# Kernel optimization log

Measured on AMD Instinct MI355X. Metric: run time of the kernel, lower is better.

## Reference

```python
import jax, jax.numpy as jnp
import numpy as np

N, M = 65536, 512
CTRL = 128
IN_DIM = 128
READ_LEN = M + 6          # [M,1,1,3,1]
WRITE_LEN = 3 * M + 6     # [M,1,1,3,1,M,M]
EPS = 1e-16


def setup_inputs() -> dict:
    key = jax.random.key(0)
    ks = jax.random.split(key, 12)
    s = 0.02
    return {
        "x":   jax.random.normal(ks[0], (4, IN_DIM), jnp.float32),
        "mem": jax.random.normal(ks[1], (N, M), jnp.float32) * 0.05,
        "Wc":  jax.random.normal(ks[2], (CTRL, IN_DIM), jnp.float32) * s,
        "bc":  jnp.zeros((CTRL,), jnp.float32),
        "Wr":  jax.random.normal(ks[3], (READ_LEN, CTRL), jnp.float32) * s,
        "br":  jnp.zeros((READ_LEN,), jnp.float32),
        "Ww":  jax.random.normal(ks[4], (WRITE_LEN, CTRL), jnp.float32) * s,
        "bw":  jnp.zeros((WRITE_LEN,), jnp.float32),
        "W1":  jax.random.normal(ks[5], (200, M + CTRL), jnp.float32) * s,
        "b1":  jnp.zeros((200,), jnp.float32),
        "W2":  jax.random.normal(ks[6], (10, 200), jnp.float32) * s,
        "b2":  jnp.zeros((10,), jnp.float32),
    }


def _address(mem, k, beta, g, s, gamma, w_prev):
    # content + gate + circular shift + sharpen (standard NTM addressing)
    beta = jax.nn.softplus(beta)
    g = jax.nn.sigmoid(g)
    s = jax.nn.softmax(s)                      # (3,)
    gamma = 1.0 + jax.nn.softplus(gamma)
    # cosine similarity against all N memory rows
    dot = mem @ k                              # (N,)
    norms = jnp.sqrt(jnp.sum(mem * mem, axis=1)) * jnp.sqrt(jnp.sum(k * k)) + EPS
    wc = jax.nn.softmax(beta * dot / norms)    # content weights (N,)
    wg = g * wc + (1.0 - g) * w_prev           # gated
    # circular convolution with 3-tap shift kernel s = [s(-1), s(0), s(+1)]
    ws = s[0] * jnp.roll(wg, 1) + s[1] * wg + s[2] * jnp.roll(wg, -1)
    w = ws ** gamma                            # sharpen
    return w / (jnp.sum(w) + EPS)


def _forward(x, mem, Wc, bc, Wr, br, Ww, bw, W1, b1, W2, b2):
    cont = x @ Wc.T + bc                       # controller: (4, 128)
    w0 = jnp.full((N,), 1.0 / N, x.dtype)      # softmax of constant -> uniform

    def step(carry, c_t):
        mem, w_r, w_w = carry
        # ---- write head ----
        ow = c_t @ Ww.T + bw                   # (3M+6,)
        k, b, g, s, y = ow[:M], ow[M], ow[M+1], ow[M+2:M+5], ow[M+5]
        e, a = ow[M+6:2*M+6], ow[2*M+6:]
        w_w = _address(mem, k, b, g, s, y, w_w)
        e = jax.nn.sigmoid(e)
        mem = mem * (1.0 - jnp.outer(w_w, e)) + jnp.outer(w_w, a)
        # ---- read head ----
        orr = c_t @ Wr.T + br                  # (M+6,)
        k, b, g, s, y = orr[:M], orr[M], orr[M+1], orr[M+2:M+5], orr[M+5]
        w_r = _address(mem, k, b, g, s, y, w_r)
        r = w_r @ mem                          # (M,)
        # ---- output MLP ----
        h = jax.nn.relu(jnp.concatenate([c_t, r]) @ W1.T + b1)
        out = h @ W2.T + b2                    # (10,)
        return (mem, w_r, w_w), out

    _, outs = jax.lax.scan(step, (mem, w0, w0), cont)
    return outs                                # (4, 10)


def reference(x, mem, Wc, bc, Wr, br, Ww, bw, W1, b1, W2, b2):
    return _forward(x, mem, Wc, bc, Wr, br, Ww, bw, W1, b1, W2, b2)
```

## Files before the change

kernel.cpp:

```cpp
#include <hip/hip_runtime.h>
#include <hip/hip_cooperative_groups.h>
#include <math.h>

namespace cg = cooperative_groups;

#define NN    65536
#define CTRLD 128
#define WLEN  1542
#define RLEN  518
#define EPSF  1e-16f
#define GRIDB 1024
#define ROWSB 64
#define RPWV  16

typedef float vf2 __attribute__((ext_vector_type(2)));

struct KP {
  const float* mem0; const float* cont;
  unsigned* mem8;
  const float* kW; const float* sW; const float* eW; const float* aW;
  const float* kR; const float* sR; float* kn;
  float *dotR, *dotW, *n2v;
  float *wunW, *pSW, *wunR, *pSR;
  float *pZr, *pZw;
  float *rp, *p2, *hbuf;
  const float *W1, *b1, *W2, *b2;
  float* out;
  const float *x, *Wc, *bc, *Ww, *bw, *Wr, *br;
  float *contw, *kWw, *sWw, *eWw, *aWw, *kRw, *sRw;
};

struct SmemAll {
  float red[256];
  float big[1280];
  float zsh[4][2];
  unsigned m8[ROWSB*128];
};

__device__ __forceinline__ float softplusf_(float x){
    return x > 0.f ? x + log1pf(expf(-x)) : log1pf(expf(x));
}
__device__ __forceinline__ float sigmoidf_(float x){ return 1.f/(1.f+expf(-x)); }
__device__ __forceinline__ float dot4_(const float4& a, const float4& b){
    return a.x*b.x + a.y*b.y + a.z*b.z + a.w*b.w;
}

__device__ __forceinline__ float blockReduce256(float v, float* red){
    int t = threadIdx.x;
    red[t] = v; __syncthreads();
    for(int s = 128; s; s >>= 1){ if(t < s) red[t] += red[t+s]; __syncthreads(); }
    float r = red[0]; __syncthreads();
    return r;
}
__device__ __forceinline__ void waveReduce3(float& a, float& b, float& c){
    for(int o = 32; o; o >>= 1){
        a += __shfl_down(a,o); b += __shfl_down(b,o); c += __shfl_down(c,o);
    }
}
__device__ __forceinline__ void waveReduce1(float& a){
    for(int o = 32; o; o >>= 1) a += __shfl_down(a,o);
}

__device__ __forceinline__ void quant8(const float4& v0, const float4& v1,
                                       unsigned& q0, unsigned& q1){
    int a = __builtin_amdgcn_cvt_pk_fp8_f32(v0.x*64.f, v0.y*64.f, 0, false);
    a     = __builtin_amdgcn_cvt_pk_fp8_f32(v0.z*64.f, v0.w*64.f, a, true);
    int b = __builtin_amdgcn_cvt_pk_fp8_f32(v1.x*64.f, v1.y*64.f, 0, false);
    b     = __builtin_amdgcn_cvt_pk_fp8_f32(v1.z*64.f, v1.w*64.f, b, true);
    q0 = (unsigned)a; q1 = (unsigned)b;
}
__device__ __forceinline__ void dequant8(unsigned q0, unsigned q1,
                                         float4& v0, float4& v1){
    vf2 a = __builtin_amdgcn_cvt_pk_f32_fp8((int)q0, false);
    vf2 b = __builtin_amdgcn_cvt_pk_f32_fp8((int)q0, true);
    vf2 c = __builtin_amdgcn_cvt_pk_f32_fp8((int)q1, false);
    vf2 d = __builtin_amdgcn_cvt_pk_f32_fp8((int)q1, true);
    const float s = 1.f/64.f;
    v0 = make_float4(a.x*s, a.y*s, b.x*s, b.y*s);
    v1 = make_float4(c.x*s, c.y*s, d.x*s, d.y*s);
}

__device__ __forceinline__ void owor_phase(const KP& p, SmemAll& sm, int bid){
    float* cs = sm.big;
    int tid = threadIdx.x;
    for(int q = tid; q < 512; q += 256){
        int t = q >> 7, c = q & 127;
        float acc = p.bc[c];
        const float* xr = p.x + t*CTRLD;
        const float* wr = p.Wc + c*CTRLD;
        for(int d = 0; d < CTRLD; ++d) acc += xr[d]*wr[d];
        cs[q] = acc;
        if(bid == 0) p.contw[q] = acc;
    }
    __syncthreads();
    int idx = bid*256 + tid;
    if(idx < 4*WLEN){
        int t = idx / WLEN, o = idx % WLEN;
        float acc = p.bw[o];
        const float* cr = cs + t*CTRLD;
        const float* wr = p.Ww + o*CTRLD;
        for(int d = 0; d < CTRLD; ++d) acc += cr[d]*wr[d];
        if(o < 512)       p.kWw[t*512 + o] = acc;
        else if(o < 518)  p.sWw[t*8 + (o-512)] = acc;
        else if(o < 1030) p.eWw[t*512 + (o-518)] = sigmoidf_(acc);
        else              p.aWw[t*512 + (o-1030)] = acc;
    } else {
        int j = idx - 4*WLEN;
        if(j < 4*RLEN){
            int t = j / RLEN, o = j % RLEN;
            float acc = p.br[o];
            const float* cr = cs + t*CTRLD;
            const float* wr = p.Wr + o*CTRLD;
            for(int d = 0; d < CTRLD; ++d) acc += cr[d]*wr[d];
            if(o < 512) p.kRw[t*512 + o] = acc;
            else        p.sRw[t*8 + (o-512)] = acc;
        }
    }
    __syncthreads();
}

template<int CH, bool RP, bool UPD, bool DOTR, bool DOTW, bool CVT, bool LDSM>
__device__ __forceinline__ void sweep_phase(const KP& p, SmemAll& sm, int rstep,
    const float* kRc, const float* sRc, int knRi,
    const float* kWn, const float* sWn, int knWi)
{
    constexpr int NW = CH + (UPD ? 1 : 0);
    constexpr int NA = (NW > 0) ? NW : 1;
    int t = threadIdx.x, bid = blockIdx.x;
    float wnorm[NA];
    #pragma unroll
    for(int j = 0; j < NW; ++j){
        float s = p.pSW[j*GRIDB+t] + p.pSW[j*GRIDB+t+256]
                + p.pSW[j*GRIDB+t+512] + p.pSW[j*GRIDB+t+768];
        wnorm[j] = 1.f/(blockReduce256(s, sm.red) + EPSF);
    }
    int wave = t >> 6, lane = t & 63;
    int c0 = 2*lane, c1 = 2*lane + 1;
    float4 ev0[NA], ev1[NA], av0[NA], av1[NA];
    #pragma unroll
    for(int j = 0; j < NW; ++j){
        ev0[j] = ((const float4*)(p.eW + j*512))[c0];
        ev1[j] = ((const float4*)(p.eW + j*512))[c1];
        av0[j] = ((const float4*)(p.aW + j*512))[c0];
        av1[j] = ((const float4*)(p.aW + j*512))[c1];
    }
    float4 kra, krb, kwa, kwb;
    float betaR = 0.f, betaW = 0.f, knRv = 1.f, knWv = 1.f;
    if constexpr(DOTR){
        kra = ((const float4*)kRc)[c0]; krb = ((const float4*)kRc)[c1];
        betaR = softplusf_(sRc[0]);
        float n2 = blockReduce256(dot4_(kra,kra) + dot4_(krb,krb), sm.red);
        knRv = sqrtf(n2*0.25f);
        if(t == 0 && bid == 0) p.kn[knRi] = knRv;
    }
    if constexpr(DOTW){
        kwa = ((const float4*)kWn)[c0]; kwb = ((const float4*)kWn)[c1];
        betaW = softplusf_(sWn[0]);
        float n2 = blockReduce256(dot4_(kwa,kwa) + dot4_(kwb,kwb), sm.red);
        knWv = sqrtf(n2*0.25f);
        if(t == 0 && bid == 0) p.kn[knWi] = knWv;
    }
    float4 rpA = {0,0,0,0}, rpB = {0,0,0,0};
    float zr = 0.f, zw = 0.f;
    int row0 = bid*ROWSB + wave*RPWV;
    for(int r = 0; r < RPWV; ++r){
        int row = row0 + r;
        int lrow = wave*RPWV + r;
        float4 v0, v1;
        if constexpr(CVT){
            const float4* src = (const float4*)p.mem0;
            v0 = src[(size_t)row*128 + c0];
            v1 = src[(size_t)row*128 + c1];
        } else {
            unsigned q0, q1;
            if constexpr(LDSM){
                q0 = sm.m8[lrow*128 + 2*lane];
                q1 = sm.m8[lrow*128 + 2*lane + 1];
            } else {
                q0 = p.mem8[(size_t)row*128 + 2*lane];
                q1 = p.mem8[(size_t)row*128 + 2*lane + 1];
            }
            dequant8(q0, q1, v0, v1);
        }
        #pragma unroll
        for(int j = 0; j < CH; ++j){
            float w = p.wunW[(size_t)j*NN + row]*wnorm[j];
            v0.x = fmaf(w, fmaf(-ev0[j].x, v0.x, av0[j].x), v0.x);
            v0.y = fmaf(w, fmaf(-ev0[j].y, v0.y, av0[j].y), v0.y);
            v0.z = fmaf(w, fmaf(-ev0[j].z, v0.z, av0[j].z), v0.z);
            v0.w = fmaf(w, fmaf(-ev0[j].w, v0.w, av0[j].w), v0.w);
            v1.x = fmaf(w, fmaf(-ev1[j].x, v1.x, av1[j].x), v1.x);
            v1.y = fmaf(w, fmaf(-ev1[j].y, v1.y, av1[j].y), v1.y);
            v1.z = fmaf(w, fmaf(-ev1[j].z, v1.z, av1[j].z), v1.z);
            v1.w = fmaf(w, fmaf(-ev1[j].w, v1.w, av1[j].w), v1.w);
        }
        if constexpr(RP){
            float wr = p.wunR[(size_t)rstep*NN + row];
            rpA.x += wr*v0.x; rpA.y += wr*v0.y; rpA.z += wr*v0.z; rpA.w += wr*v0.w;
            rpB.x += wr*v1.x; rpB.y += wr*v1.y; rpB.z += wr*v1.z; rpB.w += wr*v1.w;
        }
        if constexpr(UPD){
            float w = p.wunW[(size_t)CH*NN + row]*wnorm[CH];
            v0.x = fmaf(w, fmaf(-ev0[CH].x, v0.x, av0[CH].x), v0.x);
            v0.y = fmaf(w, fmaf(-ev0[CH].y, v0.y, av0[CH].y), v0.y);
            v0.z = fmaf(w, fmaf(-ev0[CH].z, v0.z, av0[CH].z), v0.z);
            v0.w = fmaf(w, fmaf(-ev0[CH].w, v0.w, av0[CH].w), v0.w);
            v1.x = fmaf(w, fmaf(-ev1[CH].x, v1.x, av1[CH].x), v1.x);
            v1.y = fmaf(w, fmaf(-ev1[CH].y, v1.y, av1[CH].y), v1.y);
            v1.z = fmaf(w, fmaf(-ev1[CH].z, v1.z, av1[CH].z), v1.z);
            v1.w = fmaf(w, fmaf(-ev1[CH].w, v1.w, av1[CH].w), v1.w);
        }
        if constexpr(CVT){
            unsigned q0, q1;
            quant8(v0, v1, q0, q1);
            if constexpr(LDSM){
                sm.m8[lrow*128 + 2*lane]     = q0;
                sm.m8[lrow*128 + 2*lane + 1] = q1;
            } else {
                p.mem8[(size_t)row*128 + 2*lane]     = q0;
                p.mem8[(size_t)row*128 + 2*lane + 1] = q1;
            }
        }
        if constexpr(DOTR || DOTW){
            float d = 0.f, dn = 0.f;
            float n = dot4_(v0,v0) + dot4_(v1,v1);
            if constexpr(DOTR) d  = dot4_(v0,kra) + dot4_(v1,krb);
            if constexpr(DOTW) dn = dot4_(v0,kwa) + dot4_(v1,kwb);
            waveReduce3(d, dn, n);
            if(lane == 0){
                p.n2v[row] = n;
                float sn = sqrtf(n);
                if constexpr(DOTR){ p.dotR[row] = d;  zr += expf(betaR*d /(sn*knRv + EPSF)); }
                if constexpr(DOTW){ p.dotW[row] = dn; zw += expf(betaW*dn/(sn*knWv + EPSF)); }
            }
        }
    }
    if constexpr(RP){
        float* dst = p.rp + ((size_t)(bid*4 + wave))*512;
        ((float4*)dst)[c0] = rpA;
        ((float4*)dst)[c1] = rpB;
    }
    if constexpr(DOTR || DOTW){
        if(lane == 0){ sm.zsh[wave][0] = zr; sm.zsh[wave][1] = zw; }
        __syncthreads();
        if(t == 0){
            if constexpr(DOTR) p.pZr[bid] = sm.zsh[0][0]+sm.zsh[1][0]+sm.zsh[2][0]+sm.zsh[3][0];
            if constexpr(DOTW) p.pZw[bid] = sm.zsh[0][1]+sm.zsh[1][1]+sm.zsh[2][1]+sm.zsh[3][1];
        }
    }
    __syncthreads();
}

__device__ __forceinline__ void whead_phase(const KP& p, SmemAll& sm,
    const float* sV, const float* dotv, const float* pZ,
    const float* wprev, const float* pSprev, int knidx,
    float* wun, float* pSout)
{
    int t = threadIdx.x, bid = blockIdx.x;
    float z = pZ[t] + pZ[t+256] + pZ[t+512] + pZ[t+768];
    float Z = blockReduce256(z, sm.red);
    float invSp = 1.f;
    if(pSprev){
        float sp = pSprev[t] + pSprev[t+256] + pSprev[t+512] + pSprev[t+768];
        invSp = 1.f/(blockReduce256(sp, sm.red) + EPSF);
    }
    float beta  = softplusf_(sV[0]);
    float g     = sigmoidf_(sV[1]);
    float s0 = sV[2], s1 = sV[3], s2 = sV[4];
    float smx = fmaxf(s0, fmaxf(s1, s2));
    float e0 = expf(s0-smx), e1 = expf(s1-smx), e2 = expf(s2-smx);
    float es = e0+e1+e2;
    s0 = e0/es; s1 = e1/es; s2 = e2/es;
    float gamma = 1.f + softplusf_(sV[5]);
    float knv = p.kn[knidx];
    float invZ = 1.f/Z;
    float wu = 0.f;
    if(t < ROWSB){
        int i = bid*ROWSB + t;
        int im = (i-1) & (NN-1), ip = (i+1) & (NN-1);
        auto wgf = [&](int j)->float{
            float a = beta*dotv[j]/(sqrtf(p.n2v[j])*knv + EPSF);
            float pv = wprev ? wprev[j]*invSp : (1.f/NN);
            return g*expf(a)*invZ + (1.f-g)*pv;
        };
        wu = powf(s0*wgf(im) + s1*wgf(i) + s2*wgf(ip), gamma);
        wun[i] = wu;
    }
    float S = blockReduce256(wu, sm.red);
    if(t == 0) pSout[bid] = S;
}

__device__ __forceinline__ void rsum1_phase(const KP& p, float* dst){
    int t = threadIdx.x, b = blockIdx.x;
    float2 acc; acc.x = 0.f; acc.y = 0.f;
    const float2* r2 = (const float2*)p.rp;
    for(int j = 0; j < 64; ++j){
        float2 v = r2[(size_t)(b*64 + j)*256 + t];
        acc.x += v.x; acc.y += v.y;
    }
    ((float2*)dst)[b*256 + t] = acc;
}

__device__ __forceinline__ void h_phase(const KP& p, SmemAll& sm, int hb, int step,
                                        const float* p2src){
    int t = threadIdx.x;
    const float* pS = p.pSR + step*GRIDB;
    float sp = pS[t] + pS[t+256] + pS[t+512] + pS[t+768];
    float invS = 1.f/(blockReduce256(sp, sm.red) + EPSF);
    float2 acc; acc.x = 0.f; acc.y = 0.f;
    const float2* q = (const float2*)p2src;
    for(int j = 0; j < 64; ++j){
        float2 v = q[j*256 + t];
        acc.x += v.x; acc.y += v.y;
    }
    float* conc = sm.big;
    conc[128 + 2*t]     = acc.x*invS;
    conc[128 + 2*t + 1] = acc.y*invS;
    if(t < 128) conc[t] = p.cont[step*128 + t];
    __syncthreads();
    int wave = t >> 6, lane = t & 63;
    for(int ol = wave; ol < 25; ol += 4){
        int o = hb*25 + ol;
        const float* wr = p.W1 + (size_t)o*640;
        float a = 0.f;
        for(int q2 = lane; q2 < 640; q2 += 64) a += wr[q2]*conc[q2];
        waveReduce1(a);
        if(lane == 0) p.hbuf[step*200 + o] = fmaxf(a + p.b1[o], 0.f);
    }
    __syncthreads();
}

__device__ __forceinline__ void out_phase(const KP& p, int step){
    int t = threadIdx.x;
    if(t < 10){
        float a = p.b2[t];
        const float* wr = p.W2 + t*200;
        const float* h = p.hbuf + step*200;
        for(int j = 0; j < 200; ++j) a += wr[j]*h[j];
        p.out[step*10 + t] = a;
    }
}

__device__ __forceinline__ void hfull_phase(const KP& p, SmemAll& sm, int step,
                                            const float* p2src){
    int t = threadIdx.x;
    const float* pS = p.pSR + step*GRIDB;
    float sp = pS[t] + pS[t+256] + pS[t+512] + pS[t+768];
    float invS = 1.f/(blockReduce256(sp, sm.red) + EPSF);
    float2 acc; acc.x = 0.f; acc.y = 0.f;
    const float2* q = (const float2*)p2src;
    for(int j = 0; j < 64; ++j){
        float2 v = q[j*256 + t];
        acc.x += v.x; acc.y += v.y;
    }
    float* conc = sm.big;
    conc[128 + 2*t]     = acc.x*invS;
    conc[128 + 2*t + 1] = acc.y*invS;
    if(t < 128) conc[t] = p.cont[step*128 + t];
    __syncthreads();
    int wave = t >> 6, lane = t & 63;
    float* hsh = sm.big + 640;
    for(int o = wave; o < 200; o += 4){
        const float* wr = p.W1 + (size_t)o*640;
        float a = 0.f;
        for(int q2 = lane; q2 < 640; q2 += 64) a += wr[q2]*conc[q2];
        waveReduce1(a);
        if(lane == 0) hsh[o] = fmaxf(a + p.b1[o], 0.f);
    }
    __syncthreads();
    if(t < 10){
        float a = p.b2[t];
        const float* wr = p.W2 + t*200;
        for(int j = 0; j < 200; ++j) a += wr[j]*hsh[j];
        p.out[step*10 + t] = a;
    }
}

__global__ void __launch_bounds__(256, 4) k_coop(KP p){
    cg::grid_group g = cg::this_grid();
    __shared__ SmemAll sm;
    int bid = blockIdx.x;
    if(bid < 33) owor_phase(p, sm, bid);
    g.sync();
    sweep_phase<0,false,false,false,true,true,true>(p, sm, 0, nullptr,nullptr,0, p.kW, p.sW, 0);
    g.sync();
    whead_phase(p, sm, p.sW, p.dotW, p.pZw, nullptr, nullptr, 0, p.wunW, p.pSW);
    g.sync();
    sweep_phase<0,false,true,true,true,false,true>(p, sm, 0, p.kR, p.sR, 1, p.kW+512, p.sW+8, 2);
    g.sync();
    whead_phase(p, sm, p.sR, p.dotR, p.pZr, nullptr, nullptr, 1, p.wunR, p.pSR);
    whead_phase(p, sm, p.sW+8, p.dotW, p.pZw, p.wunW, p.pSW, 2, p.wunW+NN, p.pSW+GRIDB);
    g.sync();
    sweep_phase<1,true,true,true,true,false,true>(p, sm, 0, p.kR+512, p.sR+8, 3, p.kW+1024, p.sW+16, 4);
    g.sync();
    whead_phase(p, sm, p.sR+8, p.dotR, p.pZr, p.wunR, p.pSR, 3, p.wunR+NN, p.pSR+GRIDB);
    whead_phase(p, sm, p.sW+16, p.dotW, p.pZw, p.wunW+NN, p.pSW+GRIDB, 4,
                p.wunW+2*(size_t)NN, p.pSW+2*GRIDB);
    if(bid < 64) rsum1_phase(p, p.p2);
    g.sync();
    sweep_phase<2,true,true,true,true,false,true>(p, sm, 1, p.kR+1024, p.sR+16, 5, p.kW+1536, p.sW+24, 6);
    g.sync();
    whead_phase(p, sm, p.sR+16, p.dotR, p.pZr, p.wunR+NN, p.pSR+GRIDB, 5,
                p.wunR+2*(size_t)NN, p.pSR+2*GRIDB);
    whead_phase(p, sm, p.sW+24, p.dotW, p.pZw, p.wunW+2*(size_t)NN, p.pSW+2*GRIDB, 6,
                p.wunW+3*(size_t)NN, p.pSW+3*GRIDB);
    if(bid < 64) rsum1_phase(p, p.p2 + 64*512);
    if(bid >= 64 && bid < 72) h_phase(p, sm, bid-64, 0, p.p2);
    g.sync();
    sweep_phase<3,true,true,true,false,false,true>(p, sm, 2, p.kR+1536, p.sR+24, 7, nullptr,nullptr,0);
    g.sync();
    whead_phase(p, sm, p.sR+24, p.dotR, p.pZr, p.wunR+2*(size_t)NN, p.pSR+2*GRIDB, 7,
                p.wunR+3*(size_t)NN, p.pSR+3*GRIDB);
    if(bid < 64) rsum1_phase(p, p.p2);
    if(bid >= 64 && bid < 72) h_phase(p, sm, bid-64, 1, p.p2 + 64*512);
    if(bid == 72) out_phase(p, 0);
    g.sync();
    sweep_phase<4,true,false,false,false,false,true>(p, sm, 3, nullptr,nullptr,0, nullptr,nullptr,0);
    g.sync();
    if(bid < 64) rsum1_phase(p, p.p2 + 64*512);
    if(bid >= 64 && bid < 72) h_phase(p, sm, bid-64, 2, p.p2);
    if(bid == 72) out_phase(p, 1);
    g.sync();
    if(bid == 0) hfull_phase(p, sm, 3, p.p2 + 64*512);
    if(bid == 1) out_phase(p, 2);
}

__global__ void __launch_bounds__(256) g_owor(KP p){
    __shared__ SmemAll sm;
    owor_phase(p, sm, blockIdx.x);
}
__global__ void __launch_bounds__(256) g_sweepA(KP p){
    __shared__ SmemAll sm;
    sweep_phase<0,false,false,false,true,true,false>(p, sm, 0, nullptr,nullptr,0, p.kW, p.sW, 0);
}
__global__ void __launch_bounds__(256) g_sweepC0(KP p){
    __shared__ SmemAll sm;
    sweep_phase<0,false,true,true,true,false,false>(p, sm, 0, p.kR, p.sR, 1, p.kW+512, p.sW+8, 2);
}
__global__ void __launch_bounds__(256) g_sweepC1(KP p){
    __shared__ SmemAll sm;
    sweep_phase<1,true,true,true,true,false,false>(p, sm, 0, p.kR+512, p.sR+8, 3, p.kW+1024, p.sW+16, 4);
}
__global__ void __launch_bounds__(256) g_sweepC2(KP p){
    __shared__ SmemAll sm;
    sweep_phase<2,true,true,true,true,false,false>(p, sm, 1, p.kR+1024, p.sR+16, 5, p.kW+1536, p.sW+24, 6);
}
__global__ void __launch_bounds__(256) g_sweepC3(KP p){
    __shared__ SmemAll sm;
    sweep_phase<3,true,true,true,false,false,false>(p, sm, 2, p.kR+1536, p.sR+24, 7, nullptr,nullptr,0);
}
__global__ void __launch_bounds__(256) g_sweepC4(KP p){
    __shared__ SmemAll sm;
    sweep_phase<4,true,false,false,false,false,false>(p, sm, 3, nullptr,nullptr,0, nullptr,nullptr,0);
}
__global__ void __launch_bounds__(256) g_whead(KP p, const float* sV, const float* dotv,
    const float* pZ, const float* wprev, const float* pSprev, int knidx,
    float* wun, float* pSout){
    __shared__ SmemAll sm;
    whead_phase(p, sm, sV, dotv, pZ, wprev, pSprev, knidx, wun, pSout);
}
__global__ void __launch_bounds__(256) g_rsum1(KP p, float* dst){
    rsum1_phase(p, dst);
}
__global__ void __launch_bounds__(256) g_h(KP p, int step, const float* p2src){
    __shared__ SmemAll sm;
    h_phase(p, sm, blockIdx.x, step, p2src);
}
__global__ void __launch_bounds__(256) g_out(KP p, int step){
    out_phase(p, step);
}

extern "C" void kernel_launch(void* const* d_in, const int* in_sizes, int n_in,
                              void* d_out, int out_size, void* d_ws, size_t ws_size,
                              hipStream_t stream) {
    const float* x    = (const float*)d_in[0];
    const float* mem0 = (const float*)d_in[1];
    const float* Wc   = (const float*)d_in[2];
    const float* bc   = (const float*)d_in[3];
    const float* Wr   = (const float*)d_in[4];
    const float* br   = (const float*)d_in[5];
    const float* Ww   = (const float*)d_in[6];
    const float* bw   = (const float*)d_in[7];
    const float* W1   = (const float*)d_in[8];
    const float* b1   = (const float*)d_in[9];
    const float* W2   = (const float*)d_in[10];
    const float* b2   = (const float*)d_in[11];

    float* ws = (float*)d_ws;
    size_t off = 0;
    unsigned* mem8 = (unsigned*)(ws + off); off += (size_t)NN*128;
    float* wunW = ws + off; off += 4*(size_t)NN;
    float* pSW  = ws + off; off += 4*GRIDB;
    float* wunR = ws + off; off += 4*(size_t)NN;
    float* pSR  = ws + off; off += 4*GRIDB;
    float* dotR = ws + off; off += NN;
    float* dotW = ws + off; off += NN;
    float* n2v  = ws + off; off += NN;
    float* pZr  = ws + off; off += GRIDB;
    float* pZw  = ws + off; off += GRIDB;
    float* cont = ws + off; off += 512;
    float* kW   = ws + off; off += 4*512;
    float* sW   = ws + off; off += 4*8;
    float* eW   = ws + off; off += 4*512;
    float* aW   = ws + off; off += 4*512;
    float* kR   = ws + off; off += 4*512;
    float* sR   = ws + off; off += 4*8;
    float* kn   = ws + off; off += 16;
    float* rp   = ws + off; off += (size_t)4*GRIDB*512;
    float* p2   = ws + off; off += 2*64*512;
    float* hbuf = ws + off; off += 1024;

    KP P;
    P.mem0 = mem0; P.cont = cont; P.mem8 = mem8;
    P.kW = kW; P.sW = sW; P.eW = eW; P.aW = aW; P.kR = kR; P.sR = sR; P.kn = kn;
    P.dotR = dotR; P.dotW = dotW; P.n2v = n2v;
    P.wunW = wunW; P.pSW = pSW; P.wunR = wunR; P.pSR = pSR;
    P.pZr = pZr; P.pZw = pZw;
    P.rp = rp; P.p2 = p2; P.hbuf = hbuf;
    P.W1 = W1; P.b1 = b1; P.W2 = W2; P.b2 = b2;
    P.out = (float*)d_out;
    P.x = x; P.Wc = Wc; P.bc = bc; P.Ww = Ww; P.bw = bw; P.Wr = Wr; P.br = br;
    P.contw = cont; P.kWw = kW; P.sWw = sW; P.eWw = eW; P.aWw = aW;
    P.kRw = kR; P.sRw = sR;

    bool useCoop = false;
    int coopAttr = 0;
    if(hipDeviceGetAttribute(&coopAttr, hipDeviceAttributeCooperativeLaunch, 0) == hipSuccess
       && coopAttr){
        int nCU = 0, maxb = 0;
        if(hipDeviceGetAttribute(&nCU, hipDeviceAttributeMultiprocessorCount, 0) == hipSuccess
           && hipOccupancyMaxActiveBlocksPerMultiprocessor(&maxb, k_coop, 256, 0) == hipSuccess
           && (long)maxb*(long)nCU >= GRIDB){
            useCoop = true;
        }
    }
    if(useCoop){
        void* args[] = { (void*)&P };
        hipError_t e = hipLaunchCooperativeKernel((const void*)k_coop,
                           dim3(GRIDB), dim3(256), args, 0, stream);
        if(e != hipSuccess){ (void)hipGetLastError(); useCoop = false; }
    }
    if(!useCoop){
        g_owor  <<<33, 256, 0, stream>>>(P);
        g_sweepA<<<GRIDB, 256, 0, stream>>>(P);
        g_whead <<<GRIDB, 256, 0, stream>>>(P, sW, dotW, pZw, nullptr, nullptr, 0, wunW, pSW);
        g_sweepC0<<<GRIDB, 256, 0, stream>>>(P);
        g_whead <<<GRIDB, 256, 0, stream>>>(P, sR, dotR, pZr, nullptr, nullptr, 1, wunR, pSR);
        g_whead <<<GRIDB, 256, 0, stream>>>(P, sW+8, dotW, pZw, wunW, pSW, 2, wunW+NN, pSW+GRIDB);
        g_sweepC1<<<GRIDB, 256, 0, stream>>>(P);
        g_whead <<<GRIDB, 256, 0, stream>>>(P, sR+8, dotR, pZr, wunR, pSR, 3, wunR+NN, pSR+GRIDB);
        g_whead <<<GRIDB, 256, 0, stream>>>(P, sW+16, dotW, pZw, wunW+NN, pSW+GRIDB, 4,
                                            wunW+2*(size_t)NN, pSW+2*GRIDB);
        g_rsum1 <<<64, 256, 0, stream>>>(P, p2);
        g_sweepC2<<<GRIDB, 256, 0, stream>>>(P);
        g_whead <<<GRIDB, 256, 0, stream>>>(P, sR+16, dotR, pZr, wunR+NN, pSR+GRIDB, 5,
                                            wunR+2*(size_t)NN, pSR+2*GRIDB);
        g_whead <<<GRIDB, 256, 0, stream>>>(P, sW+24, dotW, pZw, wunW+2*(size_t)NN, pSW+2*GRIDB, 6,
                                            wunW+3*(size_t)NN, pSW+3*GRIDB);
        g_rsum1 <<<64, 256, 0, stream>>>(P, p2 + 64*512);
        g_h     <<<8, 256, 0, stream>>>(P, 0, p2);
        g_sweepC3<<<GRIDB, 256, 0, stream>>>(P);
        g_whead <<<GRIDB, 256, 0, stream>>>(P, sR+24, dotR, pZr, wunR+2*(size_t)NN, pSR+2*GRIDB, 7,
                                            wunR+3*(size_t)NN, pSR+3*GRIDB);
        g_rsum1 <<<64, 256, 0, stream>>>(P, p2);
        g_h     <<<8, 256, 0, stream>>>(P, 1, p2 + 64*512);
        g_out   <<<1, 256, 0, stream>>>(P, 0);
        g_sweepC4<<<GRIDB, 256, 0, stream>>>(P);
        g_rsum1 <<<64, 256, 0, stream>>>(P, p2 + 64*512);
        g_h     <<<8, 256, 0, stream>>>(P, 2, p2);
        g_out   <<<1, 256, 0, stream>>>(P, 1);
        g_h     <<<8, 256, 0, stream>>>(P, 3, p2 + 64*512);
        g_out   <<<1, 256, 0, stream>>>(P, 2);
        g_out   <<<1, 256, 0, stream>>>(P, 3);
    }
    (void)in_sizes; (void)n_in; (void)out_size; (void)ws_size;
}
```

Baseline: 381.5 us.

## Drop LDS-resident quantized memory and pre-reduce read partials per block

Removes the shared-memory copy of each block's 8-bit quantized memory rows, so every sweep reads and writes the quantized rows through global memory instead of LDS. The four per-wave read-vector partials are also summed in LDS before being stored, which cuts the rp buffer and the rsum1 work by a factor of four. This shrinks per-block LDS use, which may help occupancy or co-residency of the cooperative grid. The cost is roughly 32 MB of extra global traffic per sweep, which may or may not stay resident in the last-level cache.

```diff
diff --git a/kernel.cpp b/kernel.cpp
--- a/kernel.cpp
+++ b/kernel.cpp
@@ -32,9 +32,8 @@
 
 struct SmemAll {
   float red[256];
-  float big[1280];
+  float big[2048];
   float zsh[4][2];
-  unsigned m8[ROWSB*128];
 };
 
 __device__ __forceinline__ float softplusf_(float x){
@@ -119,7 +118,7 @@
     __syncthreads();
 }
 
-template<int CH, bool RP, bool UPD, bool DOTR, bool DOTW, bool CVT, bool LDSM>
+template<int CH, bool RP, bool UPD, bool DOTR, bool DOTW, bool CVT>
 __device__ __forceinline__ void sweep_phase(const KP& p, SmemAll& sm, int rstep,
     const float* kRc, const float* sRc, int knRi,
     const float* kWn, const float* sWn, int knWi)
@@ -165,21 +164,14 @@
     int row0 = bid*ROWSB + wave*RPWV;
     for(int r = 0; r < RPWV; ++r){
         int row = row0 + r;
-        int lrow = wave*RPWV + r;
         float4 v0, v1;
         if constexpr(CVT){
             const float4* src = (const float4*)p.mem0;
             v0 = src[(size_t)row*128 + c0];
             v1 = src[(size_t)row*128 + c1];
         } else {
-            unsigned q0, q1;
-            if constexpr(LDSM){
-                q0 = sm.m8[lrow*128 + 2*lane];
-                q1 = sm.m8[lrow*128 + 2*lane + 1];
-            } else {
-                q0 = p.mem8[(size_t)row*128 + 2*lane];
-                q1 = p.mem8[(size_t)row*128 + 2*lane + 1];
-            }
+            unsigned q0 = p.mem8[(size_t)row*128 + 2*lane];
+            unsigned q1 = p.mem8[(size_t)row*128 + 2*lane + 1];
             dequant8(q0, q1, v0, v1);
         }
         #pragma unroll
@@ -213,13 +205,8 @@
         if constexpr(CVT){
             unsigned q0, q1;
             quant8(v0, v1, q0, q1);
-            if constexpr(LDSM){
-                sm.m8[lrow*128 + 2*lane]     = q0;
-                sm.m8[lrow*128 + 2*lane + 1] = q1;
-            } else {
-                p.mem8[(size_t)row*128 + 2*lane]     = q0;
-                p.mem8[(size_t)row*128 + 2*lane + 1] = q1;
-            }
+            p.mem8[(size_t)row*128 + 2*lane]     = q0;
+            p.mem8[(size_t)row*128 + 2*lane + 1] = q1;
         }
         if constexpr(DOTR || DOTW){
             float d = 0.f, dn = 0.f;
@@ -235,18 +222,23 @@
             }
         }
     }
-    if constexpr(RP){
-        float* dst = p.rp + ((size_t)(bid*4 + wave))*512;
-        ((float4*)dst)[c0] = rpA;
-        ((float4*)dst)[c1] = rpB;
-    }
     if constexpr(DOTR || DOTW){
         if(lane == 0){ sm.zsh[wave][0] = zr; sm.zsh[wave][1] = zw; }
-        __syncthreads();
-        if(t == 0){
-            if constexpr(DOTR) p.pZr[bid] = sm.zsh[0][0]+sm.zsh[1][0]+sm.zsh[2][0]+sm.zsh[3][0];
-            if constexpr(DOTW) p.pZw[bid] = sm.zsh[0][1]+sm.zsh[1][1]+sm.zsh[2][1]+sm.zsh[3][1];
-        }
+    }
+    if constexpr(RP){
+        ((float4*)(sm.big + wave*512))[c0] = rpA;
+        ((float4*)(sm.big + wave*512))[c1] = rpB;
+    }
+    __syncthreads();
+    if constexpr(RP){
+        p.rp[(size_t)bid*512 + t] =
+            sm.big[t] + sm.big[512+t] + sm.big[1024+t] + sm.big[1536+t];
+        p.rp[(size_t)bid*512 + t + 256] =
+            sm.big[t+256] + sm.big[768+t] + sm.big[1280+t] + sm.big[1792+t];
+    }
+    if(t == 0){
+        if constexpr(DOTR) p.pZr[bid] = sm.zsh[0][0]+sm.zsh[1][0]+sm.zsh[2][0]+sm.zsh[3][0];
+        if constexpr(DOTW) p.pZw[bid] = sm.zsh[0][1]+sm.zsh[1][1]+sm.zsh[2][1]+sm.zsh[3][1];
     }
     __syncthreads();
 }
@@ -294,8 +286,8 @@
     int t = threadIdx.x, b = blockIdx.x;
     float2 acc; acc.x = 0.f; acc.y = 0.f;
     const float2* r2 = (const float2*)p.rp;
-    for(int j = 0; j < 64; ++j){
-        float2 v = r2[(size_t)(b*64 + j)*256 + t];
+    for(int j = 0; j < 16; ++j){
+        float2 v = r2[(size_t)(b*16 + j)*256 + t];
         acc.x += v.x; acc.y += v.y;
     }
     ((float2*)dst)[b*256 + t] = acc;
@@ -382,23 +374,23 @@
     int bid = blockIdx.x;
     if(bid < 33) owor_phase(p, sm, bid);
     g.sync();
-    sweep_phase<0,false,false,false,true,true,true>(p, sm, 0, nullptr,nullptr,0, p.kW, p.sW, 0);
+    sweep_phase<0,false,false,false,true,true>(p, sm, 0, nullptr,nullptr,0, p.kW, p.sW, 0);
     g.sync();
     whead_phase(p, sm, p.sW, p.dotW, p.pZw, nullptr, nullptr, 0, p.wunW, p.pSW);
     g.sync();
-    sweep_phase<0,false,true,true,true,false,true>(p, sm, 0, p.kR, p.sR, 1, p.kW+512, p.sW+8, 2);
+    sweep_phase<0,false,true,true,true,false>(p, sm, 0, p.kR, p.sR, 1, p.kW+512, p.sW+8, 2);
     g.sync();
     whead_phase(p, sm, p.sR, p.dotR, p.pZr, nullptr, nullptr, 1, p.wunR, p.pSR);
     whead_phase(p, sm, p.sW+8, p.dotW, p.pZw, p.wunW, p.pSW, 2, p.wunW+NN, p.pSW+GRIDB);
     g.sync();
-    sweep_phase<1,true,true,true,true,false,true>(p, sm, 0, p.kR+512, p.sR+8, 3, p.kW+1024, p.sW+16, 4);
+    sweep_phase<1,true,true,true,true,false>(p, sm, 0, p.kR+512, p.sR+8, 3, p.kW+1024, p.sW+16, 4);
     g.sync();
     whead_phase(p, sm, p.sR+8, p.dotR, p.pZr, p.wunR, p.pSR, 3, p.wunR+NN, p.pSR+GRIDB);
     whead_phase(p, sm, p.sW+16, p.dotW, p.pZw, p.wunW+NN, p.pSW+GRIDB, 4,
                 p.wunW+2*(size_t)NN, p.pSW+2*GRIDB);
     if(bid < 64) rsum1_phase(p, p.p2);
     g.sync();
-    sweep_phase<2,true,true,true,true,false,true>(p, sm, 1, p.kR+1024, p.sR+16, 5, p.kW+1536, p.sW+24, 6);
+    sweep_phase<2,true,true,true,true,false>(p, sm, 1, p.kR+1024, p.sR+16, 5, p.kW+1536, p.sW+24, 6);
     g.sync();
     whead_phase(p, sm, p.sR+16, p.dotR, p.pZr, p.wunR+NN, p.pSR+GRIDB, 5,
                 p.wunR+2*(size_t)NN, p.pSR+2*GRIDB);
@@ -407,7 +399,7 @@
     if(bid < 64) rsum1_phase(p, p.p2 + 64*512);
     if(bid >= 64 && bid < 72) h_phase(p, sm, bid-64, 0, p.p2);
     g.sync();
-    sweep_phase<3,true,true,true,false,false,true>(p, sm, 2, p.kR+1536, p.sR+24, 7, nullptr,nullptr,0);
+    sweep_phase<3,true,true,true,false,false>(p, sm, 2, p.kR+1536, p.sR+24, 7, nullptr,nullptr,0);
     g.sync();
     whead_phase(p, sm, p.sR+24, p.dotR, p.pZr, p.wunR+2*(size_t)NN, p.pSR+2*GRIDB, 7,
                 p.wunR+3*(size_t)NN, p.pSR+3*GRIDB);
@@ -415,7 +407,7 @@
     if(bid >= 64 && bid < 72) h_phase(p, sm, bid-64, 1, p.p2 + 64*512);
     if(bid == 72) out_phase(p, 0);
     g.sync();
-    sweep_phase<4,true,false,false,false,false,true>(p, sm, 3, nullptr,nullptr,0, nullptr,nullptr,0);
+    sweep_phase<4,true,false,false,false,false>(p, sm, 3, nullptr,nullptr,0, nullptr,nullptr,0);
     g.sync();
     if(bid < 64) rsum1_phase(p, p.p2 + 64*512);
     if(bid >= 64 && bid < 72) h_phase(p, sm, bid-64, 2, p.p2);
@@ -431,27 +423,27 @@
 }
 __global__ void __launch_bounds__(256) g_sweepA(KP p){
     __shared__ SmemAll sm;
-    sweep_phase<0,false,false,false,true,true,false>(p, sm, 0, nullptr,nullptr,0, p.kW, p.sW, 0);
+    sweep_phase<0,false,false,false,true,true>(p, sm, 0, nullptr,nullptr,0, p.kW, p.sW, 0);
 }
 __global__ void __launch_bounds__(256) g_sweepC0(KP p){
     __shared__ SmemAll sm;
-    sweep_phase<0,false,true,true,true,false,false>(p, sm, 0, p.kR, p.sR, 1, p.kW+512, p.sW+8, 2);
+    sweep_phase<0,false,true,true,true,false>(p, sm, 0, p.kR, p.sR, 1, p.kW+512, p.sW+8, 2);
 }
 __global__ void __launch_bounds__(256) g_sweepC1(KP p){
     __shared__ SmemAll sm;
-    sweep_phase<1,true,true,true,true,false,false>(p, sm, 0, p.kR+512, p.sR+8, 3, p.kW+1024, p.sW+16, 4);
+    sweep_phase<1,true,true,true,true,false>(p, sm, 0, p.kR+512, p.sR+8, 3, p.kW+1024, p.sW+16, 4);
 }
 __global__ void __launch_bounds__(256) g_sweepC2(KP p){
     __shared__ SmemAll sm;
-    sweep_phase<2,true,true,true,true,false,false>(p, sm, 1, p.kR+1024, p.sR+16, 5, p.kW+1536, p.sW+24, 6);
+    sweep_phase<2,true,true,true,true,false>(p, sm, 1, p.kR+1024, p.sR+16, 5, p.kW+1536, p.sW+24, 6);
 }
 __global__ void __launch_bounds__(256) g_sweepC3(KP p){
     __shared__ SmemAll sm;
-    sweep_phase<3,true,true,true,false,false,false>(p, sm, 2, p.kR+1536, p.sR+24, 7, nullptr,nullptr,0);
+    sweep_phase<3,true,true,true,false,false>(p, sm, 2, p.kR+1536, p.sR+24, 7, nullptr,nullptr,0);
 }
 __global__ void __launch_bounds__(256) g_sweepC4(KP p){
     __shared__ SmemAll sm;
-    sweep_phase<4,true,false,false,false,false,false>(p, sm, 3, nullptr,nullptr,0, nullptr,nullptr,0);
+    sweep_phase<4,true,false,false,false,false>(p, sm, 3, nullptr,nullptr,0, nullptr,nullptr,0);
 }
 __global__ void __launch_bounds__(256) g_whead(KP p, const float* sV, const float* dotv,
     const float* pZ, const float* wprev, const float* pSprev, int knidx,
@@ -506,7 +498,7 @@
     float* kR   = ws + off; off += 4*512;
     float* sR   = ws + off; off += 4*8;
     float* kn   = ws + off; off += 16;
-    float* rp   = ws + off; off += (size_t)4*GRIDB*512;
+    float* rp   = ws + off; off += (size_t)GRIDB*512;
     float* p2   = ws + off; off += 2*64*512;
     float* hbuf = ws + off; off += 1024;
 
```

Result: faster. 367.1 us (-3.8%).
